# Kernel optimization log

Measured on AMD Instinct MI355X. Metric: run time of the kernel, lower is better.

The kernel has to match this reference:

```python
import jax, jax.numpy as jnp
import numpy as np

EPS = 1e-6
H = 12  # heads

def layernorm(x, alpha, bias):
    # Faithful to source: unbiased std (ddof=1) and division by (std + eps)
    mean = jnp.mean(x, axis=-1, keepdims=True)
    std = jnp.std(x, axis=-1, ddof=1, keepdims=True)
    return alpha * (x - mean) / (std + EPS) + bias

def setup_inputs() -> dict:
    key = jax.random.key(0)
    ks = jax.random.split(key, 8)
    B, S, D, F = 2, 2048, 768, 3072
    w_scale = 0.02  # keep activations in a sane range
    return {
        "x": jax.random.normal(ks[0], (B, S, D), dtype=jnp.float32),
        "src_mask": jnp.ones((B, 1, 1, S), dtype=jnp.int32),
        "wq": jax.random.normal(ks[1], (D, D), dtype=jnp.float32) * w_scale,
        "wk": jax.random.normal(ks[2], (D, D), dtype=jnp.float32) * w_scale,
        "wv": jax.random.normal(ks[3], (D, D), dtype=jnp.float32) * w_scale,
        "wo": jax.random.normal(ks[4], (D, D), dtype=jnp.float32) * w_scale,
        "w1": jax.random.normal(ks[5], (D, F), dtype=jnp.float32) * w_scale,
        "b1": jnp.zeros((F,), dtype=jnp.float32),
        "w2": jax.random.normal(ks[6], (F, D), dtype=jnp.float32) * w_scale,
        "b2": jnp.zeros((D,), dtype=jnp.float32),
        "ln1_alpha": jnp.ones((1,), dtype=jnp.float32),
        "ln1_bias": jnp.zeros((1,), dtype=jnp.float32),
        "ln2_alpha": jnp.ones((1,), dtype=jnp.float32),
        "ln2_bias": jnp.zeros((1,), dtype=jnp.float32),
    }

def reference(x, src_mask, wq, wk, wv, wo, w1, b1, w2, b2,
              ln1_alpha, ln1_bias, ln2_alpha, ln2_bias):
    B, S, D = x.shape
    dk = D // H
    # ---- residual 1: pre-LN self-attention ----
    t = layernorm(x, ln1_alpha, ln1_bias)
    q = (t @ wq).reshape(B, S, H, dk).transpose(0, 2, 1, 3)  # [B,H,S,dk]
    k = (t @ wk).reshape(B, S, H, dk).transpose(0, 2, 1, 3)
    v = (t @ wv).reshape(B, S, H, dk).transpose(0, 2, 1, 3)
    scores = jnp.einsum('bhqd,bhkd->bhqk', q, k) / jnp.sqrt(jnp.float32(dk))
    # Faithful to source quirk: masked positions are SET to 1e-9 (not -inf)
    scores = jnp.where(src_mask == 0, jnp.float32(1e-9), scores)
    attn = jax.nn.softmax(scores, axis=-1)
    o = jnp.einsum('bhqk,bhkd->bhqd', attn, v)
    o = o.transpose(0, 2, 1, 3).reshape(B, S, D) @ wo
    x = x + o
    # ---- residual 2: pre-LN FFN ----
    t = layernorm(x, ln2_alpha, ln2_bias)
    ffn = jax.nn.relu(t @ w1 + b1) @ w2 + b2
    return x + ffn
```

## Files before the change

### kernel.cpp

```cpp
#include <hip/hip_runtime.h>

typedef float f32x4 __attribute__((ext_vector_type(4)));
typedef __bf16 bf16x8 __attribute__((ext_vector_type(8)));

__device__ __forceinline__ unsigned short f2bf(float f) {
    union { float f; unsigned u; } v; v.f = f;
    unsigned r = v.u + 0x7fffu + ((v.u >> 16) & 1u);
    return (unsigned short)(r >> 16);
}

#define AS1 __attribute__((address_space(1)))
#define AS3 __attribute__((address_space(3)))
__device__ __forceinline__ void async16(const void* g, void* l) {
    __builtin_amdgcn_global_load_lds((AS1 void*)g, (AS3 void*)l, 16, 0, 0);
}

__device__ __forceinline__ void sync_lds() {
    asm volatile("s_waitcnt lgkmcnt(0)\n\ts_barrier" ::: "memory");
}

#define SWZ4(r) ((((r) & 3) ^ (((r) >> 2) & 3)))

__global__ void transpose_cvt(const float* __restrict__ W, unsigned short* __restrict__ Wt,
                              int K, int N) {
    __shared__ float tile[32][33];
    int n0 = blockIdx.x * 32, k0 = blockIdx.y * 32;
    int tx = threadIdx.x, ty = threadIdx.y;
#pragma unroll
    for (int i = 0; i < 32; i += 8)
        tile[ty + i][tx] = W[(size_t)(k0 + ty + i) * N + n0 + tx];
    __syncthreads();
#pragma unroll
    for (int i = 0; i < 32; i += 8)
        Wt[(size_t)(n0 + ty + i) * K + k0 + tx] = f2bf(tile[tx][ty + i]);
}

__global__ __launch_bounds__(256) void ln_kernel(const float* __restrict__ x,
                                                 unsigned short* __restrict__ t,
                                                 const float* __restrict__ alpha,
                                                 const float* __restrict__ bias) {
    const int row = blockIdx.x;
    const float* xr = x + (size_t)row * 768;
    float v[3], sum = 0.f, ss = 0.f;
#pragma unroll
    for (int i = 0; i < 3; i++) {
        v[i] = xr[threadIdx.x + 256 * i];
        sum += v[i]; ss += v[i] * v[i];
    }
#pragma unroll
    for (int off = 32; off; off >>= 1) {
        sum += __shfl_down(sum, off);
        ss  += __shfl_down(ss, off);
    }
    __shared__ float s1[4], s2[4];
    int wid = threadIdx.x >> 6, lane = threadIdx.x & 63;
    if (lane == 0) { s1[wid] = sum; s2[wid] = ss; }
    __syncthreads();
    if (threadIdx.x == 0) {
        float a = 0.f, b = 0.f;
#pragma unroll
        for (int i = 0; i < 4; i++) { a += s1[i]; b += s2[i]; }
        s1[0] = a; s2[0] = b;
    }
    __syncthreads();
    sum = s1[0]; ss = s2[0];
    float mean = sum * (1.f / 768.f);
    float var = (ss - sum * mean) * (1.f / 767.f);
    float sc = alpha[0] / (sqrtf(fmaxf(var, 0.f)) + 1e-6f);
    float bs = bias[0];
#pragma unroll
    for (int i = 0; i < 3; i++)
        t[(size_t)row * 768 + threadIdx.x + 256 * i] = f2bf(sc * (v[i] - mean) + bs);
}

template <int MODE>
__global__ __launch_bounds__(256, 3) void gemm_bt(
    const unsigned short* __restrict__ A, const unsigned short* __restrict__ Bt,
    int M, int N, int K, const float* __restrict__ bias,
    const float* __restrict__ res, void* __restrict__ outp) {
    __shared__ __align__(16) unsigned short As[2][128 * 32];
    __shared__ __align__(16) unsigned short Bs[2][128 * 32];
    const int tid = threadIdx.x;
    const int lane = tid & 63, w = tid >> 6;
    const int wm = w & 1, wn = w >> 1;
    const int m0 = blockIdx.y * 128, n0 = blockIdx.x * 128;
    const int quad = lane >> 4, l16 = lane & 15;

    const int r0 = tid >> 2, g0 = tid & 3;
    const int r1 = r0 + 64, g1 = g0;
    const unsigned short* gA0 = A  + (size_t)(m0 + r0) * K + g0 * 8;
    const unsigned short* gA1 = A  + (size_t)(m0 + r1) * K + g1 * 8;
    const unsigned short* gB0 = Bt + (size_t)(n0 + r0) * K + g0 * 8;
    const unsigned short* gB1 = Bt + (size_t)(n0 + r1) * K + g1 * 8;
    const int wA0 = r0 * 32 + ((g0 ^ SWZ4(r0)) * 8);
    const int wA1 = r1 * 32 + ((g1 ^ SWZ4(r1)) * 8);

    f32x4 acc[4][4];
    const f32x4 z = {0.f, 0.f, 0.f, 0.f};
#pragma unroll
    for (int mt = 0; mt < 4; mt++)
#pragma unroll
        for (int nt = 0; nt < 4; nt++) acc[mt][nt] = z;

    bf16x8 ra0 = *(const bf16x8*)gA0, ra1 = *(const bf16x8*)gA1;
    bf16x8 rb0 = *(const bf16x8*)gB0, rb1 = *(const bf16x8*)gB1;
    gA0 += 32; gA1 += 32; gB0 += 32; gB1 += 32;

    const int nK = K >> 5;
    for (int kt = 0; kt < nK; ++kt) {
        unsigned short* Ac = As[kt & 1];
        unsigned short* Bc = Bs[kt & 1];
        *(bf16x8*)&Ac[wA0] = ra0; *(bf16x8*)&Ac[wA1] = ra1;
        *(bf16x8*)&Bc[wA0] = rb0; *(bf16x8*)&Bc[wA1] = rb1;
        if (kt + 1 < nK) {
            ra0 = *(const bf16x8*)gA0; ra1 = *(const bf16x8*)gA1;
            rb0 = *(const bf16x8*)gB0; rb1 = *(const bf16x8*)gB1;
            gA0 += 32; gA1 += 32; gB0 += 32; gB1 += 32;
        }
        sync_lds();
        bf16x8 af[4], bf[4];
#pragma unroll
        for (int mt = 0; mt < 4; mt++) {
            int r = 64 * wm + 16 * mt + l16;
            af[mt] = *(const bf16x8*)&Ac[r * 32 + ((quad ^ SWZ4(r)) * 8)];
        }
#pragma unroll
        for (int nt = 0; nt < 4; nt++) {
            int r = 64 * wn + 16 * nt + l16;
            bf[nt] = *(const bf16x8*)&Bc[r * 32 + ((quad ^ SWZ4(r)) * 8)];
        }
#pragma unroll
        for (int mt = 0; mt < 4; mt++)
#pragma unroll
            for (int nt = 0; nt < 4; nt++)
                acc[mt][nt] = __builtin_amdgcn_mfma_f32_16x16x32_bf16(af[mt], bf[nt], acc[mt][nt], 0, 0, 0);
    }

#pragma unroll
    for (int mt = 0; mt < 4; mt++) {
#pragma unroll
        for (int nt = 0; nt < 4; nt++) {
            const int col = n0 + 64 * wn + 16 * nt + l16;
            float bv = 0.f;
            if (MODE == 1 || MODE == 3) bv = bias[col];
#pragma unroll
            for (int r = 0; r < 4; r++) {
                const int row = m0 + 64 * wm + 16 * mt + quad * 4 + r;
                const size_t idx = (size_t)row * N + col;
                const float v = acc[mt][nt][r];
                if (MODE == 0) ((unsigned short*)outp)[idx] = f2bf(v);
                else if (MODE == 1) ((unsigned short*)outp)[idx] = f2bf(fmaxf(v + bv, 0.f));
                else if (MODE == 2) ((float*)outp)[idx] = v + res[idx];
                else ((float*)outp)[idx] = v + bv + res[idx];
            }
        }
    }
}

template <int MODE>
__global__ __launch_bounds__(256, 3) void gemm64_bt(
    const unsigned short* __restrict__ A, const unsigned short* __restrict__ Bt,
    int M, int N, int K, const float* __restrict__ bias,
    const float* __restrict__ res, void* __restrict__ outp) {
    __shared__ __align__(16) unsigned short As[2][64 * 64];
    __shared__ __align__(16) unsigned short Bs[2][64 * 64];
    const int tid = threadIdx.x;
    const int lane = tid & 63, w = tid >> 6;
    const int m0 = blockIdx.y * 64, n0 = blockIdx.x * 64;
    const int quad = lane >> 4, l16 = lane & 15;

    const int r0 = tid >> 3, g0 = tid & 7;
    const int r1 = r0 + 32, g1 = g0;
    const unsigned short* gA0 = A  + (size_t)(m0 + r0) * K + g0 * 8;
    const unsigned short* gA1 = A  + (size_t)(m0 + r1) * K + g1 * 8;
    const unsigned short* gB0 = Bt + (size_t)(n0 + r0) * K + g0 * 8;
    const unsigned short* gB1 = Bt + (size_t)(n0 + r1) * K + g1 * 8;
    const int wA0 = r0 * 64 + ((g0 ^ (r0 & 7)) * 8);
    const int wA1 = r1 * 64 + ((g1 ^ (r1 & 7)) * 8);

    f32x4 acc[4];
    const f32x4 z = {0.f, 0.f, 0.f, 0.f};
#pragma unroll
    for (int nt = 0; nt < 4; nt++) acc[nt] = z;

    bf16x8 ra0 = *(const bf16x8*)gA0, ra1 = *(const bf16x8*)gA1;
    bf16x8 rb0 = *(const bf16x8*)gB0, rb1 = *(const bf16x8*)gB1;
    gA0 += 64; gA1 += 64; gB0 += 64; gB1 += 64;

    const int nK = K >> 6;
    for (int kt = 0; kt < nK; ++kt) {
        unsigned short* Ac = As[kt & 1];
        unsigned short* Bc = Bs[kt & 1];
        *(bf16x8*)&Ac[wA0] = ra0; *(bf16x8*)&Ac[wA1] = ra1;
        *(bf16x8*)&Bc[wA0] = rb0; *(bf16x8*)&Bc[wA1] = rb1;
        if (kt + 1 < nK) {
            ra0 = *(const bf16x8*)gA0; ra1 = *(const bf16x8*)gA1;
            rb0 = *(const bf16x8*)gB0; rb1 = *(const bf16x8*)gB1;
            gA0 += 64; gA1 += 64; gB0 += 64; gB1 += 64;
        }
        sync_lds();
        const int ra = 16 * w + l16;
        bf16x8 af0 = *(const bf16x8*)&Ac[ra * 64 + (((0 + quad) ^ (ra & 7)) * 8)];
        bf16x8 af1 = *(const bf16x8*)&Ac[ra * 64 + (((4 + quad) ^ (ra & 7)) * 8)];
#pragma unroll
        for (int nt = 0; nt < 4; nt++) {
            int rb = 16 * nt + l16;
            bf16x8 bf0 = *(const bf16x8*)&Bc[rb * 64 + (((0 + quad) ^ (rb & 7)) * 8)];
            bf16x8 bf1 = *(const bf16x8*)&Bc[rb * 64 + (((4 + quad) ^ (rb & 7)) * 8)];
            acc[nt] = __builtin_amdgcn_mfma_f32_16x16x32_bf16(af0, bf0, acc[nt], 0, 0, 0);
            acc[nt] = __builtin_amdgcn_mfma_f32_16x16x32_bf16(af1, bf1, acc[nt], 0, 0, 0);
        }
    }

#pragma unroll
    for (int nt = 0; nt < 4; nt++) {
        const int col = n0 + 16 * nt + l16;
        float bv = 0.f;
        if (MODE == 1 || MODE == 3) bv = bias[col];
#pragma unroll
        for (int rr = 0; rr < 4; rr++) {
            const int row = m0 + 16 * w + quad * 4 + rr;
            const size_t idx = (size_t)row * N + col;
            const float v = acc[nt][rr];
            if (MODE == 0) ((unsigned short*)outp)[idx] = f2bf(v);
            else if (MODE == 1) ((unsigned short*)outp)[idx] = f2bf(fmaxf(v + bv, 0.f));
            else if (MODE == 2) ((float*)outp)[idx] = v + res[idx];
            else ((float*)outp)[idx] = v + bv + res[idx];
        }
    }
}

__global__ void v_transpose(const unsigned short* __restrict__ qkvc,
                            unsigned short* __restrict__ vt) {
    __shared__ unsigned short t[64][65];
    const int bh = blockIdx.y, b = bh / 12, h = bh % 12;
    const int s0 = blockIdx.x * 64;
    const int tx = threadIdx.x, ty = threadIdx.y;
#pragma unroll
    for (int i = 0; i < 64; i += 4)
        t[ty + i][tx] = qkvc[(size_t)(b * 2048 + s0 + ty + i) * 2304 + 1536 + h * 64 + tx];
    __syncthreads();
#pragma unroll
    for (int i = 0; i < 64; i += 4)
        vt[((size_t)bh * 64 + ty + i) * 2048 + s0 + tx] = t[tx][ty + i];
}

__global__ __launch_bounds__(256, 2) void flash_attn(
    const unsigned short* __restrict__ qkvc,
    const unsigned short* __restrict__ vt,
    const int* __restrict__ mask,
    unsigned short* __restrict__ attno) {
    const int bh = blockIdx.y, b = bh / 12, h = bh % 12;
    const int s0 = blockIdx.x * 64;
    __shared__ __align__(16) unsigned short UQP[4 * 64 * 40];
    __shared__ __align__(16) unsigned short Ks[128 * 64];
    __shared__ __align__(16) unsigned short Vs[64 * 128];
    __shared__ int Ms[128];
    const int tid = threadIdx.x, lane = tid & 63, w = tid >> 6;
    const int quad = lane >> 4, l16 = lane & 15;

    {
        int sl0 = (2 * w) * 64 + lane;
        int r0 = sl0 >> 3, g0 = sl0 & 7;
        int sl1 = sl0 + 64;
        int r1 = sl1 >> 3, g1 = sl1 & 7;
        async16(qkvc + (size_t)(b * 2048 + s0 + r0) * 2304 + h * 64 + ((g0 ^ (r0 & 7)) * 8),
                UQP + (2 * w) * 512);
        async16(qkvc + (size_t)(b * 2048 + s0 + r1) * 2304 + h * 64 + ((g1 ^ (r1 & 7)) * 8),
                UQP + (2 * w + 1) * 512);
    }
    __syncthreads();
    bf16x8 aQ[4][2];
#pragma unroll
    for (int mt = 0; mt < 4; mt++) {
        int r = 16 * mt + l16;
#pragma unroll
        for (int kk = 0; kk < 2; kk++)
            aQ[mt][kk] = *(const bf16x8*)&UQP[r * 64 + (((kk * 4 + quad) ^ (r & 7)) * 8)];
    }
    __bf16* Ps = (__bf16*)UQP + w * (64 * 40);

    f32x4 Oacc[4][4], Lacc[4];
    const f32x4 z = {0.f, 0.f, 0.f, 0.f};
#pragma unroll
    for (int mt = 0; mt < 4; mt++) {
        Lacc[mt] = z;
#pragma unroll
        for (int nt = 0; nt < 4; nt++) Oacc[mt][nt] = z;
    }
    bf16x8 ones;
#pragma unroll
    for (int i = 0; i < 8; i++) ones[i] = (__bf16)1.0f;

    const unsigned short* kbase = qkvc + 768;
    const unsigned short* vbase = vt + (size_t)bh * 64 * 2048;
    const float SCL = 0.125f * 1.44269504088896340736f;
    const float MSK = 1.4426950408889634e-9f;

    for (int j = 0; j < 16; j++) {
        const int k0 = j * 128;
        __syncthreads();
#pragma unroll
        for (int c = 0; c < 4; c++) {
            int sl = (4 * w + c) * 64 + lane;
            int r = sl >> 3, g = sl & 7;
            async16(kbase + (size_t)(b * 2048 + k0 + r) * 2304 + h * 64 + ((g ^ (r & 7)) * 8),
                    Ks + (4 * w + c) * 512);
        }
#pragma unroll
        for (int c = 0; c < 4; c++) {
            int sl = (4 * w + c) * 64 + lane;
            int r = sl >> 4, g = sl & 15;
            async16(vbase + (size_t)r * 2048 + k0 + ((g ^ (r & 15)) * 8),
                    Vs + (4 * w + c) * 512);
        }
        if (tid < 128) Ms[tid] = mask[b * 2048 + k0 + tid];
        __syncthreads();

        bf16x8 bk[2][2];
        int mk[2];
#pragma unroll
        for (int nt = 0; nt < 2; nt++) {
            const int rr = w * 32 + nt * 16 + l16;
            bk[nt][0] = *(const bf16x8*)&Ks[rr * 64 + (((0 + quad) ^ (rr & 7)) * 8)];
            bk[nt][1] = *(const bf16x8*)&Ks[rr * 64 + (((4 + quad) ^ (rr & 7)) * 8)];
            mk[nt] = Ms[w * 32 + nt * 16 + l16];
        }
#pragma unroll
        for (int mt = 0; mt < 4; mt++) {
#pragma unroll
            for (int nt = 0; nt < 2; nt++) {
                f32x4 t0 = __builtin_amdgcn_mfma_f32_16x16x32_bf16(aQ[mt][0], bk[nt][0], z, 0, 0, 0);
                f32x4 sc = __builtin_amdgcn_mfma_f32_16x16x32_bf16(aQ[mt][1], bk[nt][1], t0, 0, 0, 0);
                const float fs = mk[nt] ? SCL : 0.f;
                const float ad = mk[nt] ? 0.f : MSK;
#pragma unroll
                for (int r = 0; r < 4; r++)
                    Ps[(mt * 16 + quad * 4 + r) * 40 + nt * 16 + l16] =
                        (__bf16)__builtin_amdgcn_exp2f(fmaf(sc[r], fs, ad));
            }
        }
        bf16x8 bv[4];
#pragma unroll
        for (int nt = 0; nt < 4; nt++) {
            const int rr = nt * 16 + l16;
            bv[nt] = *(const bf16x8*)&Vs[rr * 128 + (((w * 4 + quad) ^ (rr & 15)) * 8)];
        }
#pragma unroll
        for (int mt = 0; mt < 4; mt++) {
            bf16x8 aP = *(const bf16x8*)&Ps[(mt * 16 + l16) * 40 + quad * 8];
            Lacc[mt] = __builtin_amdgcn_mfma_f32_16x16x32_bf16(aP, ones, Lacc[mt], 0, 0, 0);
#pragma unroll
            for (int nt = 0; nt < 4; nt++)
                Oacc[mt][nt] = __builtin_amdgcn_mfma_f32_16x16x32_bf16(aP, bv[nt], Oacc[mt][nt], 0, 0, 0);
        }
    }

    __syncthreads();
    float* Osc = (float*)Ks;
    float* Lsc = (float*)Vs;
    if (l16 == 0) {
#pragma unroll
        for (int mt = 0; mt < 4; mt++)
#pragma unroll
            for (int r = 0; r < 4; r++)
                Lsc[w * 64 + mt * 16 + quad * 4 + r] = Lacc[mt][r];
    }
#pragma unroll
    for (int mt = 0; mt < 4; mt++) {
#pragma unroll
        for (int nt = 0; nt < 4; nt++)
#pragma unroll
            for (int r = 0; r < 4; r++)
                Osc[(w * 16 + quad * 4 + r) * 64 + nt * 16 + l16] = Oacc[mt][nt][r];
        __syncthreads();
#pragma unroll
        for (int r2 = 0; r2 < 4; r2++) {
            const int lrow = w * 4 + r2;
            float s = Osc[lrow * 64 + lane] + Osc[1024 + lrow * 64 + lane]
                    + Osc[2048 + lrow * 64 + lane] + Osc[3072 + lrow * 64 + lane];
            float L = Lsc[mt * 16 + lrow] + Lsc[64 + mt * 16 + lrow]
                    + Lsc[128 + mt * 16 + lrow] + Lsc[192 + mt * 16 + lrow];
            const int row = s0 + mt * 16 + lrow;
            attno[(size_t)(b * 2048 + row) * 768 + h * 64 + lane] = f2bf(s / L);
        }
        __syncthreads();
    }
}

extern "C" void kernel_launch(void* const* d_in, const int* in_sizes, int n_in,
                              void* d_out, int out_size, void* d_ws, size_t ws_size,
                              hipStream_t stream) {
    const float* x    = (const float*)d_in[0];
    const int*   mask = (const int*)d_in[1];
    const float* wq   = (const float*)d_in[2];
    const float* wk   = (const float*)d_in[3];
    const float* wv   = (const float*)d_in[4];
    const float* wo   = (const float*)d_in[5];
    const float* w1   = (const float*)d_in[6];
    const float* b1   = (const float*)d_in[7];
    const float* w2   = (const float*)d_in[8];
    const float* b2   = (const float*)d_in[9];
    const float* ln1a = (const float*)d_in[10];
    const float* ln1b = (const float*)d_in[11];
    const float* ln2a = (const float*)d_in[12];
    const float* ln2b = (const float*)d_in[13];

    char* p = (char*)d_ws;
    auto carve = [&](size_t bytes) {
        char* q = p;
        p += (bytes + 255) & ~(size_t)255;
        return q;
    };
    unsigned short* wTqkv = (unsigned short*)carve((size_t)2304 * 768 * 2);
    unsigned short* wTo   = (unsigned short*)carve((size_t)768 * 768 * 2);
    unsigned short* wT1   = (unsigned short*)carve((size_t)3072 * 768 * 2);
    unsigned short* wT2   = (unsigned short*)carve((size_t)768 * 3072 * 2);
    unsigned short* vtb   = (unsigned short*)carve((size_t)24 * 64 * 2048 * 2);
    float*          x1    = (float*)carve((size_t)4096 * 768 * 4);
    char* unionA = carve((size_t)4096 * 768 * 2 + (size_t)4096 * 2304 * 2);
    unsigned short* t1   = (unsigned short*)unionA;
    unsigned short* qkvc = (unsigned short*)(unionA + (size_t)4096 * 768 * 2);
    unsigned short* ffnh = (unsigned short*)unionA;
    unsigned short* attno = (unsigned short*)carve((size_t)4096 * 768 * 2);
    unsigned short* t2 = attno;

    dim3 tb(32, 8);
    transpose_cvt<<<dim3(24, 24), tb, 0, stream>>>(wq, wTqkv, 768, 768);
    transpose_cvt<<<dim3(24, 24), tb, 0, stream>>>(wk, wTqkv + (size_t)768 * 768, 768, 768);
    transpose_cvt<<<dim3(24, 24), tb, 0, stream>>>(wv, wTqkv + (size_t)1536 * 768, 768, 768);
    transpose_cvt<<<dim3(24, 24), tb, 0, stream>>>(wo, wTo, 768, 768);
    transpose_cvt<<<dim3(96, 24), tb, 0, stream>>>(w1, wT1, 768, 3072);
    transpose_cvt<<<dim3(24, 96), tb, 0, stream>>>(w2, wT2, 3072, 768);

    ln_kernel<<<4096, 256, 0, stream>>>(x, t1, ln1a, ln1b);
    gemm_bt<0><<<dim3(18, 32), 256, 0, stream>>>(t1, wTqkv, 4096, 2304, 768,
                                                 nullptr, nullptr, qkvc);
    v_transpose<<<dim3(32, 24), dim3(64, 4), 0, stream>>>(qkvc, vtb);
    flash_attn<<<dim3(32, 24), 256, 0, stream>>>(qkvc, vtb, mask, attno);
    gemm64_bt<2><<<dim3(12, 64), 256, 0, stream>>>(attno, wTo, 4096, 768, 768,
                                                   nullptr, x, x1);
    ln_kernel<<<4096, 256, 0, stream>>>(x1, t2, ln2a, ln2b);
    gemm_bt<1><<<dim3(24, 32), 256, 0, stream>>>(t2, wT1, 4096, 3072, 768,
                                                 b1, nullptr, ffnh);
    gemm64_bt<3><<<dim3(12, 64), 256, 0, stream>>>(ffnh, wT2, 4096, 768, 3072,
                                                   b2, x1, (float*)d_out);
}
```

Measured before the change: 291.8 us.

## Load K/V tiles directly into registers with prefetch instead of LDS staging

The flash attention kernel no longer stages K, V and mask tiles through shared memory. Each wave now loads exactly the K rows, V slices and mask values it needs straight from global memory into registers, and prefetches the next 128-key tile while computing the current one. This removes two block barriers per iteration and about 16 KB of LDS. The output reduction scratch is moved into the reused Q/P buffer. The trade-off is less coalesced, strided global loads and more registers held for the double buffer.

Result: no change. 289.7 us (-0.7%).

```diff
diff --git a/kernel.cpp b/kernel.cpp
--- a/kernel.cpp
+++ b/kernel.cpp
@@ -253,9 +253,6 @@
     const int bh = blockIdx.y, b = bh / 12, h = bh % 12;
     const int s0 = blockIdx.x * 64;
     __shared__ __align__(16) unsigned short UQP[4 * 64 * 40];
-    __shared__ __align__(16) unsigned short Ks[128 * 64];
-    __shared__ __align__(16) unsigned short Vs[64 * 128];
-    __shared__ int Ms[128];
     const int tid = threadIdx.x, lane = tid & 63, w = tid >> 6;
     const int quad = lane >> 4, l16 = lane & 15;
 
@@ -278,7 +275,18 @@
         for (int kk = 0; kk < 2; kk++)
             aQ[mt][kk] = *(const bf16x8*)&UQP[r * 64 + (((kk * 4 + quad) ^ (r & 7)) * 8)];
     }
+    __syncthreads();
     __bf16* Ps = (__bf16*)UQP + w * (64 * 40);
+
+    const unsigned short* kp0 = qkvc + (size_t)(b * 2048 + w * 32 + l16) * 2304
+                                + 768 + h * 64 + quad * 8;
+    const unsigned short* kp1 = kp0 + (size_t)16 * 2304;
+    const unsigned short* vp0 = vt + (size_t)bh * 64 * 2048 + (size_t)l16 * 2048
+                                + (w * 4 + quad) * 8;
+    const unsigned short* vp1 = vp0 + 16 * 2048;
+    const unsigned short* vp2 = vp0 + 32 * 2048;
+    const unsigned short* vp3 = vp0 + 48 * 2048;
+    const int* mp = mask + b * 2048 + w * 32 + l16;
 
     f32x4 Oacc[4][4], Lacc[4];
     const f32x4 z = {0.f, 0.f, 0.f, 0.f};
@@ -292,73 +300,63 @@
 #pragma unroll
     for (int i = 0; i < 8; i++) ones[i] = (__bf16)1.0f;
 
-    const unsigned short* kbase = qkvc + 768;
-    const unsigned short* vbase = vt + (size_t)bh * 64 * 2048;
     const float SCL = 0.125f * 1.44269504088896340736f;
     const float MSK = 1.4426950408889634e-9f;
 
+    bf16x8 ck[2][2], cv[4];
+    int cm[2];
+    ck[0][0] = *(const bf16x8*)kp0;       ck[0][1] = *(const bf16x8*)(kp0 + 32);
+    ck[1][0] = *(const bf16x8*)kp1;       ck[1][1] = *(const bf16x8*)(kp1 + 32);
+    cv[0] = *(const bf16x8*)vp0;  cv[1] = *(const bf16x8*)vp1;
+    cv[2] = *(const bf16x8*)vp2;  cv[3] = *(const bf16x8*)vp3;
+    cm[0] = mp[0];  cm[1] = mp[16];
+
+#pragma unroll 1
     for (int j = 0; j < 16; j++) {
-        const int k0 = j * 128;
-        __syncthreads();
-#pragma unroll
-        for (int c = 0; c < 4; c++) {
-            int sl = (4 * w + c) * 64 + lane;
-            int r = sl >> 3, g = sl & 7;
-            async16(kbase + (size_t)(b * 2048 + k0 + r) * 2304 + h * 64 + ((g ^ (r & 7)) * 8),
-                    Ks + (4 * w + c) * 512);
-        }
-#pragma unroll
-        for (int c = 0; c < 4; c++) {
-            int sl = (4 * w + c) * 64 + lane;
-            int r = sl >> 4, g = sl & 15;
-            async16(vbase + (size_t)r * 2048 + k0 + ((g ^ (r & 15)) * 8),
-                    Vs + (4 * w + c) * 512);
-        }
-        if (tid < 128) Ms[tid] = mask[b * 2048 + k0 + tid];
-        __syncthreads();
-
-        bf16x8 bk[2][2];
-        int mk[2];
-#pragma unroll
-        for (int nt = 0; nt < 2; nt++) {
-            const int rr = w * 32 + nt * 16 + l16;
-            bk[nt][0] = *(const bf16x8*)&Ks[rr * 64 + (((0 + quad) ^ (rr & 7)) * 8)];
-            bk[nt][1] = *(const bf16x8*)&Ks[rr * 64 + (((4 + quad) ^ (rr & 7)) * 8)];
-            mk[nt] = Ms[w * 32 + nt * 16 + l16];
-        }
+        bf16x8 nk[2][2], nv[4];
+        int nm[2];
+        if (j + 1 < 16) {
+            kp0 += (size_t)128 * 2304;  kp1 += (size_t)128 * 2304;
+            vp0 += 128;  vp1 += 128;  vp2 += 128;  vp3 += 128;  mp += 128;
+            nk[0][0] = *(const bf16x8*)kp0;   nk[0][1] = *(const bf16x8*)(kp0 + 32);
+            nk[1][0] = *(const bf16x8*)kp1;   nk[1][1] = *(const bf16x8*)(kp1 + 32);
+            nv[0] = *(const bf16x8*)vp0;  nv[1] = *(const bf16x8*)vp1;
+            nv[2] = *(const bf16x8*)vp2;  nv[3] = *(const bf16x8*)vp3;
+            nm[0] = mp[0];  nm[1] = mp[16];
+        }
+
 #pragma unroll
         for (int mt = 0; mt < 4; mt++) {
 #pragma unroll
             for (int nt = 0; nt < 2; nt++) {
-                f32x4 t0 = __builtin_amdgcn_mfma_f32_16x16x32_bf16(aQ[mt][0], bk[nt][0], z, 0, 0, 0);
-                f32x4 sc = __builtin_amdgcn_mfma_f32_16x16x32_bf16(aQ[mt][1], bk[nt][1], t0, 0, 0, 0);
-                const float fs = mk[nt] ? SCL : 0.f;
-                const float ad = mk[nt] ? 0.f : MSK;
+                f32x4 t0 = __builtin_amdgcn_mfma_f32_16x16x32_bf16(aQ[mt][0], ck[nt][0], z, 0, 0, 0);
+                f32x4 sc = __builtin_amdgcn_mfma_f32_16x16x32_bf16(aQ[mt][1], ck[nt][1], t0, 0, 0, 0);
+                const float fs = cm[nt] ? SCL : 0.f;
+                const float ad = cm[nt] ? 0.f : MSK;
 #pragma unroll
                 for (int r = 0; r < 4; r++)
                     Ps[(mt * 16 + quad * 4 + r) * 40 + nt * 16 + l16] =
                         (__bf16)__builtin_amdgcn_exp2f(fmaf(sc[r], fs, ad));
             }
         }
-        bf16x8 bv[4];
-#pragma unroll
-        for (int nt = 0; nt < 4; nt++) {
-            const int rr = nt * 16 + l16;
-            bv[nt] = *(const bf16x8*)&Vs[rr * 128 + (((w * 4 + quad) ^ (rr & 15)) * 8)];
-        }
 #pragma unroll
         for (int mt = 0; mt < 4; mt++) {
             bf16x8 aP = *(const bf16x8*)&Ps[(mt * 16 + l16) * 40 + quad * 8];
             Lacc[mt] = __builtin_amdgcn_mfma_f32_16x16x32_bf16(aP, ones, Lacc[mt], 0, 0, 0);
 #pragma unroll
             for (int nt = 0; nt < 4; nt++)
-                Oacc[mt][nt] = __builtin_amdgcn_mfma_f32_16x16x32_bf16(aP, bv[nt], Oacc[mt][nt], 0, 0, 0);
-        }
-    }
-
-    __syncthreads();
-    float* Osc = (float*)Ks;
-    float* Lsc = (float*)Vs;
+                Oacc[mt][nt] = __builtin_amdgcn_mfma_f32_16x16x32_bf16(aP, cv[nt], Oacc[mt][nt], 0, 0, 0);
+        }
+
+        ck[0][0] = nk[0][0]; ck[0][1] = nk[0][1];
+        ck[1][0] = nk[1][0]; ck[1][1] = nk[1][1];
+        cv[0] = nv[0]; cv[1] = nv[1]; cv[2] = nv[2]; cv[3] = nv[3];
+        cm[0] = nm[0]; cm[1] = nm[1];
+    }
+
+    __syncthreads();
+    float* Osc = (float*)UQP;
+    float* Lsc = (float*)((char*)UQP + 16384);
     if (l16 == 0) {
 #pragma unroll
         for (int mt = 0; mt < 4; mt++)
```
